# Kernel optimization log

Measured on AMD Instinct MI355X. Metric: run time of the kernel, lower is better.

Reference implementation:

```python
import jax, jax.numpy as jnp
import numpy as np

# --- Cl(5,0) geometric algebra with 32 basis blades (bitmask representation) ---
def _cayley():
    def sgn(a, b):
        # sign from reordering basis vectors (Euclidean metric: no metric signs)
        a >>= 1
        s = 0
        while a:
            s += bin(a & b).count('1')
            a >>= 1
        return -1.0 if (s & 1) else 1.0
    C = np.zeros((32, 32, 32), np.float32)
    for i in range(32):
        for j in range(32):
            C[i, j, i ^ j] = sgn(i, j)
    return jnp.asarray(C)

CAYLEY = _cayley()  # [32,32,32] structure constants
EPS = 1e-8

def geometric_product(a, b):
    # a, b: [..., 32]
    return jnp.einsum('...i,...j,ijk->...k', a, b, CAYLEY)

def manifold_normalization(x):
    # project multivector back to the unit-norm manifold
    return x * jax.lax.rsqrt(jnp.sum(x * x, axis=-1, keepdims=True) + EPS)


def setup_inputs() -> dict:
    key = jax.random.key(0)
    k1, k2, k3 = jax.random.split(key, 3)
    B, S, N, D = 16, 256, 16, 6
    H = 16  # hidden_channels
    x = jax.random.normal(k1, (B, S, N, D), dtype=jnp.float32)
    W_in = jax.random.normal(k2, (D, H * 32), dtype=jnp.float32) * 0.1
    b_in = jnp.zeros((H * 32,), dtype=jnp.float32)
    W_out = jax.random.normal(k3, (H * 32, D), dtype=jnp.float32) * 0.05
    b_out = jnp.zeros((D,), dtype=jnp.float32)
    return {"x": x, "W_in": W_in, "b_in": b_in, "W_out": W_out, "b_out": b_out}


def reference(x, W_in, b_in, W_out, b_out):
    B, S, N, D = x.shape
    H = W_in.shape[1] // 32
    # proj_in over the whole sequence at once
    x_embs = (x @ W_in + b_in).reshape(B, S, N, H, 32)
    # psi init: identity rotor (scalar blade = 1)
    psi0 = jnp.zeros((B, N, H, 32), dtype=x.dtype).at[..., 0].set(1.0)

    def step(psi, inp):
        u_t, x_t = inp  # [B,N,H,32], [B,N,D]
        delta_r = manifold_normalization(u_t.at[..., 0].add(1.0))
        psi = manifold_normalization(geometric_product(delta_r, psi))
        pred_delta = psi.reshape(B, N, H * 32) @ W_out + b_out
        return psi, x_t + pred_delta

    _, ys = jax.lax.scan(step, psi0,
                         (jnp.swapaxes(x_embs, 0, 1), jnp.swapaxes(x, 0, 1)))
    return jnp.swapaxes(ys, 0, 1)  # [B,S,N,D]
```

## Files before the change

### kernel.cpp

```cpp
#include <hip/hip_runtime.h>


#define EPS 1e-8f

constexpr int pcnt(int v) { int s = 0; while (v) { s += v & 1; v >>= 1; } return s; }
constexpr float sgnf(int a, int b) {
    a >>= 1; int s = 0;
    while (a) { s += pcnt(a & b); a >>= 1; }
    return (s & 1) ? -1.0f : 1.0f;
}
struct Tab16 {
    float sg2[16][16];
    float sig[16];
    int   cm[16];
};
constexpr Tab16 make16() {
    Tab16 t{};
    for (int c = 0; c < 16; ++c) {
        int m = c | ((pcnt(c) & 1) << 4);
        t.cm[c] = m;
        t.sig[c] = sgnf(m ^ 31, 31);
    }
    for (int i = 0; i < 16; ++i)
        for (int j = 0; j < 16; ++j)
            t.sg2[i][j] = sgnf(t.cm[i], t.cm[j]);
    return t;
}
__device__ constexpr Tab16 T16 = make16();

__global__ __launch_bounds__(256, 1) void k_prep(
        const float* __restrict__ W_in, const float* __restrict__ b_in,
        float* __restrict__ WP) {
    const int idx = blockIdx.x * 256 + threadIdx.x;
    if (idx >= 16 * 224) return;
    const int h = idx / 224, r = idx % 224;
    const int sg = r / 112, r2 = r % 112;
    const float pm = sg ? -1.0f : 1.0f;
    float val;
    if (r2 < 96) {
        const int d = r2 >> 4, c = r2 & 15, m = T16.cm[c];
        val = W_in[d * 512 + h * 32 + m]
            + pm * T16.sig[c] * W_in[d * 512 + h * 32 + (m ^ 31)];
    } else {
        const int c = r2 - 96, m = T16.cm[c];
        val = b_in[h * 32 + m] + pm * T16.sig[c] * b_in[h * 32 + (m ^ 31)];
    }
    WP[idx] = val;
}

__device__ __forceinline__ void build_u16(const float* __restrict__ Wsp,
                                          const float xv[6], float U[16]) {
#pragma unroll
    for (int c = 0; c < 16; ++c) U[c] = Wsp[96 + c];
#pragma unroll
    for (int d = 0; d < 6; ++d)
#pragma unroll
        for (int c = 0; c < 16; ++c)
            U[c] = fmaf(xv[d], Wsp[d * 16 + c], U[c]);
    U[0] += 1.0f;
}

__device__ __forceinline__ void gp16(float* __restrict__ np,
                                     const float* __restrict__ U,
                                     const float* __restrict__ R) {
#pragma unroll
    for (int c1 = 0; c1 < 16; ++c1)
#pragma unroll
        for (int c2 = 0; c2 < 16; ++c2)
            np[c1 ^ c2] = fmaf(T16.sg2[c1][c2] * U[c1], R[c2], np[c1 ^ c2]);
}

__device__ __forceinline__ float ssum32(const float* a, const float* b) {
    float s0 = 0.f, s1 = 0.f, s2 = 0.f, s3 = 0.f;
#pragma unroll
    for (int k = 0; k < 16; k += 4) {
        s0 = fmaf(a[k],     a[k],     s0); s1 = fmaf(a[k + 1], a[k + 1], s1);
        s2 = fmaf(a[k + 2], a[k + 2], s2); s3 = fmaf(a[k + 3], a[k + 3], s3);
        s0 = fmaf(b[k],     b[k],     s0); s1 = fmaf(b[k + 1], b[k + 1], s1);
        s2 = fmaf(b[k + 2], b[k + 2], s2); s3 = fmaf(b[k + 3], b[k + 3], s3);
    }
    return (s0 + s1) + (s2 + s3);
}

__global__ __launch_bounds__(256, 1) void k_fused(
        const float* __restrict__ x, const float* __restrict__ WP,
        const float* __restrict__ W_out, float* __restrict__ WS4) {
    __shared__ float LP[4 * 8 * 64 * 6];

    const int tid  = threadIdx.x;
    const int lane = tid & 63;
    const int w    = __builtin_amdgcn_readfirstlane((int)(tid >> 6));
    const int hg   = blockIdx.x & 3;
    const int p    = blockIdx.x >> 2;
    const int h    = 4 * hg + w;
    const int sc   = lane & 31;
    const int bn = p * 2 + (lane >> 5), b = bn >> 4, n = bn & 15;
    const float* __restrict__ Wp0 = WP + h * 224;
    const float* __restrict__ Wp1 = WP + h * 224 + 112;
    const float* __restrict__ Oh  = W_out + h * 192;

    float Ap[16], Am[16];
    {
        const int t = sc * 8;
        const float2* xp = (const float2*)(x + ((b * 256 + t) * 16 + n) * 6);
        float2 x01 = xp[0], x23 = xp[1], x45 = xp[2];
        const float xv[6] = {x01.x, x01.y, x23.x, x23.y, x45.x, x45.y};
        build_u16(Wp0, xv, Ap);
        build_u16(Wp1, xv, Am);
    }
    for (int i = 1; i < 8; ++i) {
        const int t = sc * 8 + i;
        const float2* xp = (const float2*)(x + ((b * 256 + t) * 16 + n) * 6);
        float2 x01 = xp[0], x23 = xp[1], x45 = xp[2];
        const float xv[6] = {x01.x, x01.y, x23.x, x23.y, x45.x, x45.y};
        float U[16], np[16];
        build_u16(Wp0, xv, U);
#pragma unroll
        for (int k = 0; k < 16; ++k) np[k] = 0.0f;
        gp16(np, U, Ap);
#pragma unroll
        for (int k = 0; k < 16; ++k) Ap[k] = np[k];
        build_u16(Wp1, xv, U);
#pragma unroll
        for (int k = 0; k < 16; ++k) np[k] = 0.0f;
        gp16(np, U, Am);
#pragma unroll
        for (int k = 0; k < 16; ++k) Am[k] = np[k];
    }
    {
        float rs = rsqrtf(0.5f * ssum32(Ap, Am) + EPS);
#pragma unroll
        for (int k = 0; k < 16; ++k) { Ap[k] *= rs; Am[k] *= rs; }
    }

#pragma unroll
    for (int k = 1; k < 32; k <<= 1) {
        float prp[16], prm[16];
#pragma unroll
        for (int j = 0; j < 16; ++j) {
            prp[j] = __shfl_up(Ap[j], k, 32);
            prm[j] = __shfl_up(Am[j], k, 32);
        }
        if (sc >= k) {
            float np[16];
#pragma unroll
            for (int m = 0; m < 16; ++m) np[m] = 0.0f;
            gp16(np, Ap, prp);
#pragma unroll
            for (int m = 0; m < 16; ++m) Ap[m] = np[m];
#pragma unroll
            for (int m = 0; m < 16; ++m) np[m] = 0.0f;
            gp16(np, Am, prm);
#pragma unroll
            for (int m = 0; m < 16; ++m) Am[m] = np[m];
        }
    }
    {
        float rs = rsqrtf(0.5f * ssum32(Ap, Am) + EPS);
#pragma unroll
        for (int j = 0; j < 16; ++j) { Ap[j] *= rs; Am[j] *= rs; }
    }
    float Rp[16], Rm[16];
#pragma unroll
    for (int j = 0; j < 16; ++j) {
        Rp[j] = __shfl_up(Ap[j], 1, 32);
        Rm[j] = __shfl_up(Am[j], 1, 32);
    }
    if (sc == 0) {
#pragma unroll
        for (int j = 0; j < 16; ++j) { Rp[j] = 0.0f; Rm[j] = 0.0f; }
        Rp[0] = 1.0f; Rm[0] = 1.0f;
    }

    for (int i = 0; i < 8; ++i) {
        const int t = sc * 8 + i;
        const float2* xp = (const float2*)(x + ((b * 256 + t) * 16 + n) * 6);
        float2 x01 = xp[0], x23 = xp[1], x45 = xp[2];
        const float xv[6] = {x01.x, x01.y, x23.x, x23.y, x45.x, x45.y};
        float U[16], npp[16], npm[16];
        build_u16(Wp0, xv, U);
#pragma unroll
        for (int k = 0; k < 16; ++k) npp[k] = 0.0f;
        gp16(npp, U, Rp);
        build_u16(Wp1, xv, U);
#pragma unroll
        for (int k = 0; k < 16; ++k) npm[k] = 0.0f;
        gp16(npm, U, Rm);
        float rs = 0.5f * rsqrtf(0.5f * ssum32(npp, npm) + EPS);
        float pd[6] = {0.f, 0.f, 0.f, 0.f, 0.f, 0.f};
#pragma unroll
        for (int c = 0; c < 16; ++c) {
            const int m = T16.cm[c];
            const float ev = npp[c] + npm[c];
            const float od = T16.sig[c] * (npp[c] - npm[c]);
#pragma unroll
            for (int d = 0; d < 6; ++d) {
                pd[d] = fmaf(ev, Oh[m * 6 + d], pd[d]);
                pd[d] = fmaf(od, Oh[(m ^ 31) * 6 + d], pd[d]);
            }
        }
#pragma unroll
        for (int k = 0; k < 16; ++k) { Rp[k] = npp[k]; Rm[k] = npm[k]; }
        float* lp = LP + ((w * 8 + i) * 64 + lane) * 6;
#pragma unroll
        for (int d = 0; d < 6; ++d) lp[d] = pd[d] * rs;
    }

    __syncthreads();

    float* outp = WS4 + (hg * 128 + p) * 3072;
    for (int s = tid; s < 3072; s += 256) {
        const int d = s % 6, tc = s / 6;
        const int c = tc & 1, t = tc >> 1;
        const int li = ((t & 7) * 64 + (c * 32 + (t >> 3))) * 6 + d;
        float acc = LP[0 * 3072 + li] + LP[1 * 3072 + li]
                  + LP[2 * 3072 + li] + LP[3 * 3072 + li];
        outp[s] = acc;
    }
}

__global__ __launch_bounds__(256, 1) void k_reduce(
        const float* __restrict__ x, const float* __restrict__ b_out,
        const float* __restrict__ WS4, float* __restrict__ out) {
    const int idx = blockIdx.x * 256 + threadIdx.x;
    const int p = idx / 3072, s = idx % 3072;
    const int d = s % 6, tc = s / 6;
    const int c = tc & 1, t = tc >> 1;
    const int bn = p * 2 + c, b = bn >> 4, n = bn & 15;
    const int o = ((b * 256 + t) * 16 + n) * 6 + d;
    float acc = x[o] + b_out[d];
#pragma unroll
    for (int hg = 0; hg < 4; ++hg)
        acc += WS4[(hg * 128 + p) * 3072 + s];
    out[o] = acc;
}

extern "C" void kernel_launch(void* const* d_in, const int* in_sizes, int n_in,
                              void* d_out, int out_size, void* d_ws, size_t ws_size,
                              hipStream_t stream) {
    (void)in_sizes; (void)n_in; (void)out_size; (void)ws_size;
    const float* x     = (const float*)d_in[0];
    const float* W_in  = (const float*)d_in[1];
    const float* b_in  = (const float*)d_in[2];
    const float* W_out = (const float*)d_in[3];
    const float* b_out = (const float*)d_in[4];
    float* out = (float*)d_out;

    float* WP  = (float*)d_ws;
    float* WS4 = (float*)((char*)d_ws + 16384);

    k_prep  <<<14,   256, 0, stream>>>(W_in, b_in, WP);
    k_fused <<<512,  256, 0, stream>>>(x, WP, W_out, WS4);
    k_reduce<<<1536, 256, 0, stream>>>(x, b_out, WS4, out);
}
```

Before: 134.7 us.

## Represent even Cl(5,0) halves as 2x2 quaternion matrices to cut product cost

Replaces the 16x16 signed even-subalgebra geometric product with a block form that uses the isomorphism to 2x2 quaternion matrices. Each product becomes eight quaternion multiply-accumulates, 128 FMAs with no sign-table multiplies, where the old code did 256 FMAs plus sign scaling. The input projection is re-expressed in the new basis, and the output projection is also folded into that basis in the prep kernel so the epilogue skips the even/odd recombination. The prep kernel grows and the normalization constants change. Correctness depends on the compile-time derivation checked by static_assert.

```diff
diff --git a/kernel.cpp b/kernel.cpp
--- a/kernel.cpp
+++ b/kernel.cpp
@@ -4,52 +4,124 @@
 #define EPS 1e-8f
 
 constexpr int pcnt(int v) { int s = 0; while (v) { s += v & 1; v >>= 1; } return s; }
-constexpr float sgnf(int a, int b) {
+constexpr int sgni(int a, int b) {
     a >>= 1; int s = 0;
     while (a) { s += pcnt(a & b); a >>= 1; }
-    return (s & 1) ? -1.0f : 1.0f;
-}
-struct Tab16 {
-    float sg2[16][16];
-    float sig[16];
-    int   cm[16];
+    return (s & 1) ? -1 : 1;
+}
+struct El { int m; int s; };
+constexpr El emul(El a, El b) { return { a.m ^ b.m, a.s * b.s * sgni(a.m, b.m) }; }
+
+struct MTab {
+    int mm[16]; int ms[16];
+    int qi[4][4]; int qs[4][4];
+    int sig[32];
+    bool ok;
 };
-constexpr Tab16 make16() {
-    Tab16 t{};
-    for (int c = 0; c < 16; ++c) {
-        int m = c | ((pcnt(c) & 1) << 4);
-        t.cm[c] = m;
-        t.sig[c] = sgnf(m ^ 31, 31);
-    }
+constexpr MTab mkMT() {
+    MTab t{}; t.ok = true;
+    El g0{17,1}, g1{18,1}, g2{20,1}, g3{24,1};
+    El q1 = emul(g0, g1), q2 = emul(g1, g2);
+    El q[4] = { El{0,1}, q1, q2, emul(q1, q2) };
+    El u = emul(emul(g0, g1), emul(g2, g3));
+    El v = emul(emul(g0, g1), g2);
+    El mset[4] = { El{0,1}, u, v, emul(u, v) };
+    {
+        El c1 = emul(q[1], q[1]); if (!(c1.m == 0 && c1.s == -1)) t.ok = false;
+        El c2 = emul(q[2], q[2]); if (!(c2.m == 0 && c2.s == -1)) t.ok = false;
+        El c3 = emul(q[3], q[3]); if (!(c3.m == 0 && c3.s == -1)) t.ok = false;
+        El c4 = emul(u, u); if (!(c4.m == 0 && c4.s == 1)) t.ok = false;
+        El c5 = emul(v, v); if (!(c5.m == 0 && c5.s == 1)) t.ok = false;
+        El c6 = emul(u, v), c7 = emul(v, u);
+        if (!(c6.m == c7.m && c6.s == -c7.s)) t.ok = false;
+        for (int i = 1; i < 4; ++i) {
+            El a1 = emul(u, q[i]), a2 = emul(q[i], u);
+            if (!(a1.m == a2.m && a1.s == a2.s)) t.ok = false;
+            El b1 = emul(v, q[i]), b2 = emul(q[i], v);
+            if (!(b1.m == b2.m && b1.s == b2.s)) t.ok = false;
+        }
+    }
+    for (int tt = 0; tt < 4; ++tt)
+        for (int a = 0; a < 4; ++a) {
+            El e = emul(q[a], mset[tt]);
+            t.mm[a + 4 * tt] = e.m; t.ms[a + 4 * tt] = e.s;
+            if (pcnt(e.m) & 1) t.ok = false;
+        }
     for (int i = 0; i < 16; ++i)
-        for (int j = 0; j < 16; ++j)
-            t.sg2[i][j] = sgnf(t.cm[i], t.cm[j]);
+        for (int j = i + 1; j < 16; ++j)
+            if (t.mm[i] == t.mm[j]) t.ok = false;
+    for (int a = 0; a < 4; ++a)
+        for (int b = 0; b < 4; ++b) {
+            El e = emul(q[a], q[b]);
+            int f = -1;
+            for (int c = 0; c < 4; ++c) if (q[c].m == e.m) f = c;
+            if (f < 0) { t.ok = false; f = 0; }
+            t.qi[a][b] = f; t.qs[a][b] = e.s * q[f].s;
+        }
+    for (int m = 0; m < 32; ++m) t.sig[m] = sgni(m ^ 31, 31);
     return t;
 }
-__device__ constexpr Tab16 T16 = make16();
+__device__ constexpr MTab MT = mkMT();
+static_assert(mkMT().ok, "Cl(5,0) = M2(H)+M2(H) derivation failed");
 
 __global__ __launch_bounds__(256, 1) void k_prep(
         const float* __restrict__ W_in, const float* __restrict__ b_in,
-        float* __restrict__ WP) {
+        const float* __restrict__ W_out, float* __restrict__ WP) {
     const int idx = blockIdx.x * 256 + threadIdx.x;
-    if (idx >= 16 * 224) return;
-    const int h = idx / 224, r = idx % 224;
-    const int sg = r / 112, r2 = r % 112;
-    const float pm = sg ? -1.0f : 1.0f;
-    float val;
-    if (r2 < 96) {
-        const int d = r2 >> 4, c = r2 & 15, m = T16.cm[c];
-        val = W_in[d * 512 + h * 32 + m]
-            + pm * T16.sig[c] * W_in[d * 512 + h * 32 + (m ^ 31)];
+    if (idx >= 6656) return;
+    if (idx < 3584) {
+        const int h = idx / 224, r = idx % 224;
+        const int es = r / 112, r2 = r % 112;
+        const float p = es ? -1.f : 1.f;
+        const int c = (r2 < 96) ? (r2 & 15) : (r2 - 96);
+        const int e = c >> 2, a = c & 3;
+        const int base = (e == 0 || e == 3) ? 0 : 8;
+        const float se = (e == 0 || e == 1) ? 1.f : -1.f;
+        float val = 0.f;
+        for (int k = 0; k < 2; ++k) {
+            const int i = a + base + 4 * k;
+            const float beta = k ? se : 1.f;
+            const int m = MT.mm[i];
+            const float s = (float)MT.ms[i];
+            const float sg = (float)MT.sig[m];
+            float wm, wn;
+            if (r2 < 96) {
+                const int d = r2 >> 4;
+                wm = W_in[d * 512 + h * 32 + m];
+                wn = W_in[d * 512 + h * 32 + (m ^ 31)];
+            } else {
+                wm = b_in[h * 32 + m];
+                wn = b_in[h * 32 + (m ^ 31)];
+            }
+            val += beta * s * (wm + p * sg * wn);
+        }
+        WP[idx] = val;
     } else {
-        const int c = r2 - 96, m = T16.cm[c];
-        val = b_in[h * 32 + m] + pm * T16.sig[c] * b_in[h * 32 + (m ^ 31)];
-    }
-    WP[idx] = val;
-}
-
-__device__ __forceinline__ void build_u16(const float* __restrict__ Wsp,
-                                          const float xv[6], float U[16]) {
+        const int j = idx - 3584;
+        const int h = j / 192, r = j % 192;
+        const int es = r / 96, r2 = r % 96;
+        const float p = es ? -1.f : 1.f;
+        const int c = r2 / 6, d = r2 % 6;
+        const int e = c >> 2, a = c & 3;
+        const int base = (e == 0 || e == 3) ? 0 : 8;
+        const float se = (e == 0 || e == 1) ? 1.f : -1.f;
+        float val = 0.f;
+        for (int k = 0; k < 2; ++k) {
+            const int i = a + base + 4 * k;
+            const float beta = k ? se : 1.f;
+            const int m = MT.mm[i];
+            const float s = (float)MT.ms[i];
+            const float sg = (float)MT.sig[m];
+            const float wm = W_out[(h * 32 + m) * 6 + d];
+            const float wn = W_out[(h * 32 + (m ^ 31)) * 6 + d];
+            val += 0.25f * beta * s * (wm + p * sg * wn);
+        }
+        WP[idx] = val;
+    }
+}
+
+__device__ __forceinline__ void build16(const float* __restrict__ Wsp,
+                                        const float xv[6], float U[16]) {
 #pragma unroll
     for (int c = 0; c < 16; ++c) U[c] = Wsp[96 + c];
 #pragma unroll
@@ -57,17 +129,29 @@
 #pragma unroll
         for (int c = 0; c < 16; ++c)
             U[c] = fmaf(xv[d], Wsp[d * 16 + c], U[c]);
-    U[0] += 1.0f;
-}
-
-__device__ __forceinline__ void gp16(float* __restrict__ np,
-                                     const float* __restrict__ U,
-                                     const float* __restrict__ R) {
-#pragma unroll
-    for (int c1 = 0; c1 < 16; ++c1)
-#pragma unroll
-        for (int c2 = 0; c2 < 16; ++c2)
-            np[c1 ^ c2] = fmaf(T16.sg2[c1][c2] * U[c1], R[c2], np[c1 ^ c2]);
+    U[0]  += 1.0f;
+    U[12] += 1.0f;
+}
+
+__device__ __forceinline__ void hfma(float* __restrict__ z,
+                                     const float* __restrict__ p,
+                                     const float* __restrict__ q) {
+#pragma unroll
+    for (int a = 0; a < 4; ++a)
+#pragma unroll
+        for (int b = 0; b < 4; ++b)
+            z[MT.qi[a][b]] = fmaf((float)MT.qs[a][b] * p[a], q[b], z[MT.qi[a][b]]);
+}
+
+__device__ __forceinline__ void gpm(float* __restrict__ Z,
+                                    const float* __restrict__ U,
+                                    const float* __restrict__ X) {
+#pragma unroll
+    for (int k = 0; k < 16; ++k) Z[k] = 0.f;
+    hfma(Z + 0,  U + 0, X + 0);   hfma(Z + 0,  U + 4,  X + 8);
+    hfma(Z + 4,  U + 0, X + 4);   hfma(Z + 4,  U + 4,  X + 12);
+    hfma(Z + 8,  U + 8, X + 0);   hfma(Z + 8,  U + 12, X + 8);
+    hfma(Z + 12, U + 8, X + 4);   hfma(Z + 12, U + 12, X + 12);
 }
 
 __device__ __forceinline__ float ssum32(const float* a, const float* b) {
@@ -84,7 +168,7 @@
 
 __global__ __launch_bounds__(256, 1) void k_fused(
         const float* __restrict__ x, const float* __restrict__ WP,
-        const float* __restrict__ W_out, float* __restrict__ WS4) {
+        float* __restrict__ WS4) {
     __shared__ float LP[4 * 8 * 64 * 6];
 
     const int tid  = threadIdx.x;
@@ -97,40 +181,37 @@
     const int bn = p * 2 + (lane >> 5), b = bn >> 4, n = bn & 15;
     const float* __restrict__ Wp0 = WP + h * 224;
     const float* __restrict__ Wp1 = WP + h * 224 + 112;
-    const float* __restrict__ Oh  = W_out + h * 192;
-
-    float Ap[16], Am[16];
+    const float* __restrict__ Op0 = WP + 3584 + h * 192;
+    const float* __restrict__ Op1 = WP + 3584 + h * 192 + 96;
+
+    float Xp[16], Xm[16];
     {
         const int t = sc * 8;
         const float2* xp = (const float2*)(x + ((b * 256 + t) * 16 + n) * 6);
         float2 x01 = xp[0], x23 = xp[1], x45 = xp[2];
         const float xv[6] = {x01.x, x01.y, x23.x, x23.y, x45.x, x45.y};
-        build_u16(Wp0, xv, Ap);
-        build_u16(Wp1, xv, Am);
+        build16(Wp0, xv, Xp);
+        build16(Wp1, xv, Xm);
     }
     for (int i = 1; i < 8; ++i) {
         const int t = sc * 8 + i;
         const float2* xp = (const float2*)(x + ((b * 256 + t) * 16 + n) * 6);
         float2 x01 = xp[0], x23 = xp[1], x45 = xp[2];
         const float xv[6] = {x01.x, x01.y, x23.x, x23.y, x45.x, x45.y};
-        float U[16], np[16];
-        build_u16(Wp0, xv, U);
-#pragma unroll
-        for (int k = 0; k < 16; ++k) np[k] = 0.0f;
-        gp16(np, U, Ap);
-#pragma unroll
-        for (int k = 0; k < 16; ++k) Ap[k] = np[k];
-        build_u16(Wp1, xv, U);
-#pragma unroll
-        for (int k = 0; k < 16; ++k) np[k] = 0.0f;
-        gp16(np, U, Am);
-#pragma unroll
-        for (int k = 0; k < 16; ++k) Am[k] = np[k];
+        float U[16], Z[16];
+        build16(Wp0, xv, U);
+        gpm(Z, U, Xp);
+#pragma unroll
+        for (int k = 0; k < 16; ++k) Xp[k] = Z[k];
+        build16(Wp1, xv, U);
+        gpm(Z, U, Xm);
+#pragma unroll
+        for (int k = 0; k < 16; ++k) Xm[k] = Z[k];
     }
     {
-        float rs = rsqrtf(0.5f * ssum32(Ap, Am) + EPS);
-#pragma unroll
-        for (int k = 0; k < 16; ++k) { Ap[k] *= rs; Am[k] *= rs; }
+        float rs = rsqrtf(0.25f * ssum32(Xp, Xm) + EPS);
+#pragma unroll
+        for (int k = 0; k < 16; ++k) { Xp[k] *= rs; Xm[k] *= rs; }
     }
 
 #pragma unroll
@@ -138,38 +219,35 @@
         float prp[16], prm[16];
 #pragma unroll
         for (int j = 0; j < 16; ++j) {
-            prp[j] = __shfl_up(Ap[j], k, 32);
-            prm[j] = __shfl_up(Am[j], k, 32);
+            prp[j] = __shfl_up(Xp[j], k, 32);
+            prm[j] = __shfl_up(Xm[j], k, 32);
         }
         if (sc >= k) {
-            float np[16];
-#pragma unroll
-            for (int m = 0; m < 16; ++m) np[m] = 0.0f;
-            gp16(np, Ap, prp);
-#pragma unroll
-            for (int m = 0; m < 16; ++m) Ap[m] = np[m];
-#pragma unroll
-            for (int m = 0; m < 16; ++m) np[m] = 0.0f;
-            gp16(np, Am, prm);
-#pragma unroll
-            for (int m = 0; m < 16; ++m) Am[m] = np[m];
+            float Z[16];
+            gpm(Z, Xp, prp);
+#pragma unroll
+            for (int m = 0; m < 16; ++m) Xp[m] = Z[m];
+            gpm(Z, Xm, prm);
+#pragma unroll
+            for (int m = 0; m < 16; ++m) Xm[m] = Z[m];
         }
     }
     {
-        float rs = rsqrtf(0.5f * ssum32(Ap, Am) + EPS);
-#pragma unroll
-        for (int j = 0; j < 16; ++j) { Ap[j] *= rs; Am[j] *= rs; }
+        float rs = rsqrtf(0.25f * ssum32(Xp, Xm) + EPS);
+#pragma unroll
+        for (int j = 0; j < 16; ++j) { Xp[j] *= rs; Xm[j] *= rs; }
     }
     float Rp[16], Rm[16];
 #pragma unroll
     for (int j = 0; j < 16; ++j) {
-        Rp[j] = __shfl_up(Ap[j], 1, 32);
-        Rm[j] = __shfl_up(Am[j], 1, 32);
+        Rp[j] = __shfl_up(Xp[j], 1, 32);
+        Rm[j] = __shfl_up(Xm[j], 1, 32);
     }
     if (sc == 0) {
 #pragma unroll
         for (int j = 0; j < 16; ++j) { Rp[j] = 0.0f; Rm[j] = 0.0f; }
-        Rp[0] = 1.0f; Rm[0] = 1.0f;
+        Rp[0] = 1.0f; Rp[12] = 1.0f;
+        Rm[0] = 1.0f; Rm[12] = 1.0f;
     }
 
     for (int i = 0; i < 8; ++i) {
@@ -177,30 +255,22 @@
         const float2* xp = (const float2*)(x + ((b * 256 + t) * 16 + n) * 6);
         float2 x01 = xp[0], x23 = xp[1], x45 = xp[2];
         const float xv[6] = {x01.x, x01.y, x23.x, x23.y, x45.x, x45.y};
-        float U[16], npp[16], npm[16];
-        build_u16(Wp0, xv, U);
-#pragma unroll
-        for (int k = 0; k < 16; ++k) npp[k] = 0.0f;
-        gp16(npp, U, Rp);
-        build_u16(Wp1, xv, U);
-#pragma unroll
-        for (int k = 0; k < 16; ++k) npm[k] = 0.0f;
-        gp16(npm, U, Rm);
-        float rs = 0.5f * rsqrtf(0.5f * ssum32(npp, npm) + EPS);
+        float U[16], Zp[16], Zm[16];
+        build16(Wp0, xv, U);
+        gpm(Zp, U, Rp);
+        build16(Wp1, xv, U);
+        gpm(Zm, U, Rm);
+        float rs = rsqrtf(0.25f * ssum32(Zp, Zm) + EPS);
         float pd[6] = {0.f, 0.f, 0.f, 0.f, 0.f, 0.f};
 #pragma unroll
-        for (int c = 0; c < 16; ++c) {
-            const int m = T16.cm[c];
-            const float ev = npp[c] + npm[c];
-            const float od = T16.sig[c] * (npp[c] - npm[c]);
+        for (int c = 0; c < 16; ++c)
 #pragma unroll
             for (int d = 0; d < 6; ++d) {
-                pd[d] = fmaf(ev, Oh[m * 6 + d], pd[d]);
-                pd[d] = fmaf(od, Oh[(m ^ 31) * 6 + d], pd[d]);
+                pd[d] = fmaf(Zp[c], Op0[c * 6 + d], pd[d]);
+                pd[d] = fmaf(Zm[c], Op1[c * 6 + d], pd[d]);
             }
-        }
-#pragma unroll
-        for (int k = 0; k < 16; ++k) { Rp[k] = npp[k]; Rm[k] = npm[k]; }
+#pragma unroll
+        for (int k = 0; k < 16; ++k) { Rp[k] = Zp[k]; Rm[k] = Zm[k]; }
         float* lp = LP + ((w * 8 + i) * 64 + lane) * 6;
 #pragma unroll
         for (int d = 0; d < 6; ++d) lp[d] = pd[d] * rs;
@@ -247,9 +317,9 @@
     float* out = (float*)d_out;
 
     float* WP  = (float*)d_ws;
-    float* WS4 = (float*)((char*)d_ws + 16384);
-
-    k_prep  <<<14,   256, 0, stream>>>(W_in, b_in, WP);
-    k_fused <<<512,  256, 0, stream>>>(x, WP, W_out, WS4);
+    float* WS4 = (float*)((char*)d_ws + 32768);
+
+    k_prep  <<<26,   256, 0, stream>>>(W_in, b_in, W_out, WP);
+    k_fused <<<512,  256, 0, stream>>>(x, WP, WS4);
     k_reduce<<<1536, 256, 0, stream>>>(x, b_out, WS4, out);
 }
```

Result: faster. 119.4 us (-11.3%).
